# Kernel tuning notes

Hardware: AMD Instinct MI355X
Metric: run time of the kernel (lower is better)

## Reference

```python
import jax, jax.numpy as jnp
import numpy as np

B, M, D = 2048, 40, 64          # batch, num fields, embedding dim
HIDDEN = [128, 128, 128]        # CIN layer sizes


def setup_inputs() -> dict:
    key = jax.random.key(0)
    kx, k0, k1, k2 = jax.random.split(key, 4)
    x = jax.random.normal(kx, (B, M, D), dtype=jnp.float32)
    # torch.rand -> uniform [0, 1)
    W0 = jax.random.uniform(k0, (M, M, HIDDEN[0]), dtype=jnp.float32)
    W1 = jax.random.uniform(k1, (M, HIDDEN[0], HIDDEN[1]), dtype=jnp.float32)
    W2 = jax.random.uniform(k2, (M, HIDDEN[1], HIDDEN[2]), dtype=jnp.float32)
    return {"x": x, "W0": W0, "W1": W1, "W2": W2}


def _cin_forward(x, Ws):
    # x: [b, m, d]. Each layer k:
    #   x_next[b, l, d] = sum_{m, h} x0[b, m, d] * x_k[b, h, d] * W_k[m, h, l]
    # which equals the torch 'bil,bjl->bjil' outer product followed by
    # 'bijk,ijl->bkl' + transpose, but expressed as one fused contraction
    # (opt_einsum picks a path avoiding the worst intermediate).
    ps = []
    xk = x  # [b, H_k, d], H_0 = m
    for W in Ws:
        x_next = jnp.einsum('bmd,bhd,mhl->bld', x, xk, W)  # [b, L_k, d]
        ps.append(jnp.sum(x_next, axis=2))                  # [b, L_k]
        xk = x_next
    return jnp.concatenate(ps, axis=1)                      # [b, sum(L_k)]


def reference(x, W0, W1, W2):
    return _cin_forward(x, (W0, W1, W2))
```

## Files before the change

### kernel.cpp

```cpp
#include <hip/hip_runtime.h>
#include <hip/hip_bf16.h>
#include <cstdint>

#define BATCH 2048
#define MF    40
#define DDIM  64
#define LDIM  128
#define ROWS  (BATCH * DDIM)

typedef __attribute__((ext_vector_type(4)))  short    short4_t;
typedef __attribute__((ext_vector_type(8)))  short    short8;
typedef __attribute__((ext_vector_type(8)))  __bf16   bf16x8;
typedef __attribute__((ext_vector_type(4)))  float    floatx4;
typedef __attribute__((ext_vector_type(16))) float    floatx16;

__device__ __forceinline__ unsigned short f32_to_bf16(float f) {
    union { float f; uint32_t u; } v; v.f = f;
    uint32_t u = v.u;
    uint32_t r = (u + 0x7fffu + ((u >> 16) & 1u)) >> 16;
    return (unsigned short)r;
}

__device__ __forceinline__ void barrier_raw() {
    asm volatile("s_barrier" ::: "memory");
}
template <int N> __device__ __forceinline__ void vmwait() {
    if constexpr (N == 0)  asm volatile("s_waitcnt vmcnt(0)"  ::: "memory");
    if constexpr (N == 3)  asm volatile("s_waitcnt vmcnt(3)"  ::: "memory");
    if constexpr (N == 4)  asm volatile("s_waitcnt vmcnt(4)"  ::: "memory");
    if constexpr (N == 11) asm volatile("s_waitcnt vmcnt(11)" ::: "memory");
    if constexpr (N == 12) asm volatile("s_waitcnt vmcnt(12)" ::: "memory");
}

__global__ void k_wprep(const float* __restrict__ W, unsigned short* __restrict__ Wt,
                        int KK, int H) {
    int bi = blockIdx.x;
    int lane = threadIdx.x;
    int cb = bi & 3;
    int mkk = bi >> 2;
    int kk = mkk % KK, m = mkk / KK;
    int l = cb * 32 + (lane & 31);
    int hbase = kk * 16 + (lane >> 5) * 8;
    unsigned short o[8];
#pragma unroll
    for (int j = 0; j < 8; ++j) {
        int h = hbase + j;
        float v = (h < H) ? W[((size_t)m * H + h) * LDIM + l] : 0.f;
        o[j] = f32_to_bf16(v);
    }
    *(short8*)(Wt + ((size_t)bi * 64 + lane) * 8) = *(const short8*)o;
}

template <int KK, int KU, bool FIRST, int OFF, bool WRITEX>
__global__ __launch_bounds__(256, 2) void k_gemm(
    const float* __restrict__ x,
    const unsigned short* __restrict__ Xprev,
    const unsigned short* __restrict__ Wt,
    unsigned short* __restrict__ Xout,
    float* __restrict__ out)
{
    constexpr int UPM   = KK / KU;
    constexpr int NU    = MF * UPM;
    constexpr int DIST  = (KU == 4) ? 2 : 3;
    constexpr int SLOTS = (KU == 4) ? 2 : 3;

    __shared__ unsigned short slab[4][KU * 2048];

    const int tid  = threadIdx.x;
    const int lane = tid & 63, wave = tid >> 6;
    const int hf   = lane >> 5, r31 = lane & 31;
    const int rowhalf = wave >> 1, colhalf = wave & 1;
    const int b = blockIdx.x * 2 + rowhalf;

    bf16x8 afrag[2][KK];
    if constexpr (FIRST) {
#pragma unroll
        for (int t = 0; t < 2; ++t)
#pragma unroll
            for (int kk = 0; kk < KK; ++kk) {
                unsigned short tmp[8];
#pragma unroll
                for (int j = 0; j < 8; ++j) {
                    int h = kk * 16 + hf * 8 + j;
                    float v = (h < MF) ? x[((size_t)b * MF + h) * DDIM + t * 32 + r31] : 0.f;
                    tmp[j] = f32_to_bf16(v);
                }
                afrag[t][kk] = __builtin_bit_cast(bf16x8, *(const short8*)tmp);
            }
    } else {
        const int g = r31 >> 3, hs = (r31 >> 2) & 1, ii = r31 & 3;
#pragma unroll
        for (int t = 0; t < 2; ++t) {
            int tile = b * 2 + t;
#pragma unroll
            for (int kk = 0; kk < KK; ++kk) {
                int k0  = kk * 16 + hf * 8;
                int cbk = k0 >> 5, rr = k0 & 31;
                const unsigned short* p =
                    Xprev + ((size_t)(((tile * 4 + cbk) * 4 + g) * 2 + hs) * 32 + rr) * 4 + ii;
                unsigned short tmp[8];
#pragma unroll
                for (int j = 0; j < 8; ++j) tmp[j] = p[(size_t)j * 4];
                afrag[t][kk] = __builtin_bit_cast(bf16x8, *(const short8*)tmp);
            }
        }
    }

    floatx16 acc[2][2] = {};

    auto stage = [&](int uu) {
        int u = uu < NU ? uu : NU - 1;
        const unsigned short* src = Wt + (size_t)u * (KU * 2048);
#pragma unroll
        for (int it = 0; it < KU; ++it) {
            int c = it * 256 + tid;
            __builtin_amdgcn_global_load_lds(
                (const __attribute__((address_space(1))) uint32_t*)(src + (size_t)c * 8),
                (__attribute__((address_space(3))) uint32_t*)(&slab[u & 3][(size_t)c * 8]),
                16, 0, 0);
        }
    };

    const int cbg0 = colhalf * 2, cbg1 = colhalf * 2 + 1;
    auto ldfrag = [&](int u, int frag, int cb) {
        return __builtin_bit_cast(bf16x8,
            *(const short8*)(&slab[u & 3][((size_t)(frag * 4 + cb) * 64 + lane) * 8]));
    };

    vmwait<0>();
    stage(0); stage(1); stage(2);
    vmwait<(KU == 4) ? 4 : 3>();
    barrier_raw();

    bf16x8 bbuf[SLOTS][2];
#pragma unroll
    for (int p = 0; p < SLOTS; ++p) {
        bbuf[p][0] = ldfrag(0, p, cbg0);
        bbuf[p][1] = ldfrag(0, p, cbg1);
    }

    floatx4 sc0[4], sc1[4];

#pragma unroll 1
    for (int m = 0; m < MF; ++m) {
        floatx16 P[2][2] = {};
#pragma unroll
        for (int kk = 0; kk < KK; ++kk) {
            if (kk % KU == 0) {
                barrier_raw();
                if (kk == 0) {
                    const floatx4* sp4 = (const floatx4*)(x + ((size_t)b * MF + m) * DDIM);
#pragma unroll
                    for (int g = 0; g < 4; ++g) {
                        sc0[g] = sp4[hf + 2 * g];
                        sc1[g] = sp4[8 + hf + 2 * g];
                    }
                }
                stage(m * UPM + kk / KU + 3);
            }
            const int slot = (KU == 4) ? (kk & 1) : kk;
            P[0][0] = __builtin_amdgcn_mfma_f32_32x32x16_bf16(afrag[0][kk], bbuf[slot][0], P[0][0], 0, 0, 0);
            P[1][0] = __builtin_amdgcn_mfma_f32_32x32x16_bf16(afrag[1][kk], bbuf[slot][0], P[1][0], 0, 0, 0);
            P[0][1] = __builtin_amdgcn_mfma_f32_32x32x16_bf16(afrag[0][kk], bbuf[slot][1], P[0][1], 0, 0, 0);
            P[1][1] = __builtin_amdgcn_mfma_f32_32x32x16_bf16(afrag[1][kk], bbuf[slot][1], P[1][1], 0, 0, 0);
            {
                const int j  = kk + DIST;
                int mm = m + ((j >= KK) ? 1 : 0);
                if (mm > MF - 1) mm = MF - 1;
                const int jj = (j >= KK) ? (j - KK) : j;
                const int u  = mm * UPM + jj / KU;
                bbuf[slot][0] = ldfrag(u, jj % KU, cbg0);
                bbuf[slot][1] = ldfrag(u, jj % KU, cbg1);
            }
            if (kk % KU == KU - 1) {
                if (KU == 3)      vmwait<11>();
                else if (kk == 3) vmwait<12>();
                else              vmwait<4>();
            }
        }
#pragma unroll
        for (int cbp = 0; cbp < 2; ++cbp)
#pragma unroll
            for (int g = 0; g < 4; ++g)
#pragma unroll
                for (int i = 0; i < 4; ++i) {
                    acc[0][cbp][g * 4 + i] += sc0[g][i] * P[0][cbp][g * 4 + i];
                    acc[1][cbp][g * 4 + i] += sc1[g][i] * P[1][cbp][g * 4 + i];
                }
    }

    if constexpr (WRITEX) {
#pragma unroll
        for (int t = 0; t < 2; ++t) {
            int tile = b * 2 + t;
#pragma unroll
            for (int cbp = 0; cbp < 2; ++cbp) {
                int cb = colhalf * 2 + cbp;
#pragma unroll
                for (int g = 0; g < 4; ++g) {
                    unsigned short o[4];
#pragma unroll
                    for (int i = 0; i < 4; ++i) o[i] = f32_to_bf16(acc[t][cbp][g * 4 + i]);
                    *(short4_t*)(Xout +
                        ((size_t)(((tile * 4 + cb) * 4 + g) * 2 + hf) * 32 + r31) * 4) =
                        *(const short4_t*)o;
                }
            }
        }
    }

#pragma unroll
    for (int cbp = 0; cbp < 2; ++cbp) {
        float v = 0.f;
#pragma unroll
        for (int j = 0; j < 16; ++j) v += acc[0][cbp][j] + acc[1][cbp][j];
        v += __shfl_xor(v, 32);
        if (hf == 0)
            out[(size_t)b * 384 + OFF + (colhalf * 2 + cbp) * 32 + r31] = v;
    }
}

extern "C" void kernel_launch(void* const* d_in, const int* in_sizes, int n_in,
                              void* d_out, int out_size, void* d_ws, size_t ws_size,
                              hipStream_t stream) {
    const float* x  = (const float*)d_in[0];
    const float* W0 = (const float*)d_in[1];
    const float* W1 = (const float*)d_in[2];
    const float* W2 = (const float*)d_in[3];
    float* out = (float*)d_out;

    char* ws = (char*)d_ws;
    size_t off = 0;
    auto alloc = [&](size_t bytes) -> void* {
        void* p = ws + off;
        off += (bytes + 255) & ~(size_t)255;
        return p;
    };
    unsigned short* W0t = (unsigned short*)alloc((size_t)MF * 3 * 2048 * 2);
    unsigned short* W1t = (unsigned short*)alloc((size_t)MF * 8 * 2048 * 2);
    unsigned short* W2t = (unsigned short*)alloc((size_t)MF * 8 * 2048 * 2);
    unsigned short* X1p = (unsigned short*)alloc((size_t)ROWS * LDIM * 2);
    unsigned short* X2p = (unsigned short*)alloc((size_t)ROWS * LDIM * 2);

    k_wprep<<<MF * 3 * 4, 64, 0, stream>>>(W0, W0t, 3, 40);
    k_wprep<<<MF * 8 * 4, 64, 0, stream>>>(W1, W1t, 8, 128);
    k_wprep<<<MF * 8 * 4, 64, 0, stream>>>(W2, W2t, 8, 128);

    k_gemm<3, 3, true,  0,   true ><<<ROWS / 128, 256, 0, stream>>>(x, nullptr, W0t, X1p, out);
    k_gemm<8, 4, false, 128, true ><<<ROWS / 128, 256, 0, stream>>>(x, X1p,     W1t, X2p, out);
    k_gemm<8, 4, false, 256, false><<<ROWS / 128, 256, 0, stream>>>(x, X2p,     W2t, X2p, out);
}
```

Before: 460.0 us.

## Swap MFMA operands so W is A-operand, use row-major X layout

Swaps the MFMA operand order so the weight fragment is the A operand and the activation the B operand. The output tile then holds l along rows and d along lanes, so the per-field scale becomes one scalar per lane and the intermediate X can be stored and loaded row-major with 16-byte vector loads instead of strided gathers. It also adds s_setprio around the MFMA loop, unifies the prefetch distance and vmcnt waits, and uses packed float2 FMAs for the scaling. In exchange the final row sum now needs a 5-step cross-lane shuffle reduction for each of the 16 accumulator elements.

```diff
diff --git a/kernel.cpp b/kernel.cpp
--- a/kernel.cpp
+++ b/kernel.cpp
@@ -11,7 +11,7 @@
 typedef __attribute__((ext_vector_type(4)))  short    short4_t;
 typedef __attribute__((ext_vector_type(8)))  short    short8;
 typedef __attribute__((ext_vector_type(8)))  __bf16   bf16x8;
-typedef __attribute__((ext_vector_type(4)))  float    floatx4;
+typedef __attribute__((ext_vector_type(2)))  float    floatx2;
 typedef __attribute__((ext_vector_type(16))) float    floatx16;
 
 __device__ __forceinline__ unsigned short f32_to_bf16(float f) {
@@ -28,8 +28,7 @@
     if constexpr (N == 0)  asm volatile("s_waitcnt vmcnt(0)"  ::: "memory");
     if constexpr (N == 3)  asm volatile("s_waitcnt vmcnt(3)"  ::: "memory");
     if constexpr (N == 4)  asm volatile("s_waitcnt vmcnt(4)"  ::: "memory");
-    if constexpr (N == 11) asm volatile("s_waitcnt vmcnt(11)" ::: "memory");
-    if constexpr (N == 12) asm volatile("s_waitcnt vmcnt(12)" ::: "memory");
+    if constexpr (N == 10) asm volatile("s_waitcnt vmcnt(10)" ::: "memory");
 }
 
 __global__ void k_wprep(const float* __restrict__ W, unsigned short* __restrict__ Wt,
@@ -61,8 +60,8 @@
 {
     constexpr int UPM   = KK / KU;
     constexpr int NU    = MF * UPM;
-    constexpr int DIST  = (KU == 4) ? 2 : 3;
     constexpr int SLOTS = (KU == 4) ? 2 : 3;
+    constexpr int DIST  = SLOTS;
 
     __shared__ unsigned short slab[4][KU * 2048];
 
@@ -72,7 +71,7 @@
     const int rowhalf = wave >> 1, colhalf = wave & 1;
     const int b = blockIdx.x * 2 + rowhalf;
 
-    bf16x8 afrag[2][KK];
+    bf16x8 xk[2][KK];
     if constexpr (FIRST) {
 #pragma unroll
         for (int t = 0; t < 2; ++t)
@@ -85,25 +84,15 @@
                     float v = (h < MF) ? x[((size_t)b * MF + h) * DDIM + t * 32 + r31] : 0.f;
                     tmp[j] = f32_to_bf16(v);
                 }
-                afrag[t][kk] = __builtin_bit_cast(bf16x8, *(const short8*)tmp);
+                xk[t][kk] = __builtin_bit_cast(bf16x8, *(const short8*)tmp);
             }
     } else {
-        const int g = r31 >> 3, hs = (r31 >> 2) & 1, ii = r31 & 3;
-#pragma unroll
-        for (int t = 0; t < 2; ++t) {
-            int tile = b * 2 + t;
-#pragma unroll
-            for (int kk = 0; kk < KK; ++kk) {
-                int k0  = kk * 16 + hf * 8;
-                int cbk = k0 >> 5, rr = k0 & 31;
-                const unsigned short* p =
-                    Xprev + ((size_t)(((tile * 4 + cbk) * 4 + g) * 2 + hs) * 32 + rr) * 4 + ii;
-                unsigned short tmp[8];
-#pragma unroll
-                for (int j = 0; j < 8; ++j) tmp[j] = p[(size_t)j * 4];
-                afrag[t][kk] = __builtin_bit_cast(bf16x8, *(const short8*)tmp);
-            }
-        }
+#pragma unroll
+        for (int t = 0; t < 2; ++t)
+#pragma unroll
+            for (int kk = 0; kk < KK; ++kk)
+                xk[t][kk] = __builtin_bit_cast(bf16x8, *(const short8*)(
+                    Xprev + (size_t)(b * 64 + t * 32 + r31) * LDIM + kk * 16 + hf * 8));
     }
 
     floatx16 acc[2][2] = {};
@@ -139,7 +128,7 @@
         bbuf[p][1] = ldfrag(0, p, cbg1);
     }
 
-    floatx4 sc0[4], sc1[4];
+    float s0v = 0.f, s1v = 0.f;
 
 #pragma unroll 1
     for (int m = 0; m < MF; ++m) {
@@ -148,21 +137,19 @@
         for (int kk = 0; kk < KK; ++kk) {
             if (kk % KU == 0) {
                 barrier_raw();
+                asm volatile("s_setprio 1");
                 if (kk == 0) {
-                    const floatx4* sp4 = (const floatx4*)(x + ((size_t)b * MF + m) * DDIM);
-#pragma unroll
-                    for (int g = 0; g < 4; ++g) {
-                        sc0[g] = sp4[hf + 2 * g];
-                        sc1[g] = sp4[8 + hf + 2 * g];
-                    }
+                    const float* sp = x + ((size_t)b * MF + m) * DDIM + r31;
+                    s0v = sp[0];
+                    s1v = sp[32];
                 }
                 stage(m * UPM + kk / KU + 3);
             }
             const int slot = (KU == 4) ? (kk & 1) : kk;
-            P[0][0] = __builtin_amdgcn_mfma_f32_32x32x16_bf16(afrag[0][kk], bbuf[slot][0], P[0][0], 0, 0, 0);
-            P[1][0] = __builtin_amdgcn_mfma_f32_32x32x16_bf16(afrag[1][kk], bbuf[slot][0], P[1][0], 0, 0, 0);
-            P[0][1] = __builtin_amdgcn_mfma_f32_32x32x16_bf16(afrag[0][kk], bbuf[slot][1], P[0][1], 0, 0, 0);
-            P[1][1] = __builtin_amdgcn_mfma_f32_32x32x16_bf16(afrag[1][kk], bbuf[slot][1], P[1][1], 0, 0, 0);
+            P[0][0] = __builtin_amdgcn_mfma_f32_32x32x16_bf16(bbuf[slot][0], xk[0][kk], P[0][0], 0, 0, 0);
+            P[1][0] = __builtin_amdgcn_mfma_f32_32x32x16_bf16(bbuf[slot][0], xk[1][kk], P[1][0], 0, 0, 0);
+            P[0][1] = __builtin_amdgcn_mfma_f32_32x32x16_bf16(bbuf[slot][1], xk[0][kk], P[0][1], 0, 0, 0);
+            P[1][1] = __builtin_amdgcn_mfma_f32_32x32x16_bf16(bbuf[slot][1], xk[1][kk], P[1][1], 0, 0, 0);
             {
                 const int j  = kk + DIST;
                 int mm = m + ((j >= KK) ? 1 : 0);
@@ -172,37 +159,35 @@
                 bbuf[slot][0] = ldfrag(u, jj % KU, cbg0);
                 bbuf[slot][1] = ldfrag(u, jj % KU, cbg1);
             }
-            if (kk % KU == KU - 1) {
-                if (KU == 3)      vmwait<11>();
-                else if (kk == 3) vmwait<12>();
-                else              vmwait<4>();
-            }
-        }
-#pragma unroll
-        for (int cbp = 0; cbp < 2; ++cbp)
-#pragma unroll
-            for (int g = 0; g < 4; ++g)
-#pragma unroll
-                for (int i = 0; i < 4; ++i) {
-                    acc[0][cbp][g * 4 + i] += sc0[g][i] * P[0][cbp][g * 4 + i];
-                    acc[1][cbp][g * 4 + i] += sc1[g][i] * P[1][cbp][g * 4 + i];
-                }
+            if (kk % KU == KU - 1) vmwait<10>();
+        }
+        asm volatile("s_setprio 0");
+#pragma unroll
+        for (int t = 0; t < 2; ++t) {
+            const float sv = (t == 0) ? s0v : s1v;
+            floatx2 s2 = {sv, sv};
+#pragma unroll
+            for (int cbp = 0; cbp < 2; ++cbp) {
+                floatx2*       A = (floatx2*)&acc[t][cbp];
+                const floatx2* Q = (const floatx2*)&P[t][cbp];
+#pragma unroll
+                for (int i = 0; i < 8; ++i) A[i] += s2 * Q[i];
+            }
+        }
     }
 
     if constexpr (WRITEX) {
 #pragma unroll
         for (int t = 0; t < 2; ++t) {
-            int tile = b * 2 + t;
+            const size_t rowbase = (size_t)(b * 64 + t * 32 + r31) * LDIM;
 #pragma unroll
             for (int cbp = 0; cbp < 2; ++cbp) {
-                int cb = colhalf * 2 + cbp;
 #pragma unroll
                 for (int g = 0; g < 4; ++g) {
                     unsigned short o[4];
 #pragma unroll
                     for (int i = 0; i < 4; ++i) o[i] = f32_to_bf16(acc[t][cbp][g * 4 + i]);
-                    *(short4_t*)(Xout +
-                        ((size_t)(((tile * 4 + cb) * 4 + g) * 2 + hf) * 32 + r31) * 4) =
+                    *(short4_t*)(Xout + rowbase + (colhalf * 2 + cbp) * 32 + 8 * g + 4 * hf) =
                         *(const short4_t*)o;
                 }
             }
@@ -211,12 +196,18 @@
 
 #pragma unroll
     for (int cbp = 0; cbp < 2; ++cbp) {
-        float v = 0.f;
-#pragma unroll
-        for (int j = 0; j < 16; ++j) v += acc[0][cbp][j] + acc[1][cbp][j];
-        v += __shfl_xor(v, 32);
-        if (hf == 0)
-            out[(size_t)b * 384 + OFF + (colhalf * 2 + cbp) * 32 + r31] = v;
+#pragma unroll
+        for (int j = 0; j < 16; ++j) {
+            float v = acc[0][cbp][j] + acc[1][cbp][j];
+            v += __shfl_xor(v, 16);
+            v += __shfl_xor(v, 8);
+            v += __shfl_xor(v, 4);
+            v += __shfl_xor(v, 2);
+            v += __shfl_xor(v, 1);
+            if (r31 == 0)
+                out[(size_t)b * 384 + OFF + (colhalf * 2 + cbp) * 32 +
+                    (j & 3) + 8 * (j >> 2) + 4 * hf] = v;
+        }
     }
 }
 
```

New measurement: 463.2 us. Within noise of the previous version (+0.7%).
